# Kernel optimization log

Measured on AMD Instinct MI355X. Metric: run time of the kernel, lower is better.

## Reference

```python
import jax, jax.numpy as jnp
import numpy as np

N = 16384       # num_nodes
IN = 128        # in_features
OUT = 128       # out_features
E = 524288      # num edges
NG = 8          # FastKAN num_grids
GRID_MIN, GRID_MAX = -2.0, 2.0
LN_EPS = 1e-5


def setup_inputs() -> dict:
    key = jax.random.key(0)
    ks = jax.random.split(key, 6)
    x = jax.random.normal(ks[0], (N, IN), dtype=jnp.float32)
    edge_index = jax.random.randint(ks[1], (2, E), 0, N, dtype=jnp.int32)
    # FastKANLayer params
    ln_gamma = jnp.ones((IN,), jnp.float32)
    ln_beta = jnp.zeros((IN,), jnp.float32)
    # SplineLinear: trunc-normal-ish init with scale 0.1 (fast-kan default)
    spline_w = (jax.random.normal(ks[2], (OUT, IN * NG), jnp.float32)
                * (0.1 / np.sqrt(IN * NG)))
    base_w = jax.random.normal(ks[3], (OUT, IN), jnp.float32) / np.sqrt(IN)
    base_b = jnp.zeros((OUT,), jnp.float32)
    # GCNConv.bias
    bias = jax.random.normal(ks[4], (OUT,), jnp.float32) * 0.01
    return dict(x=x, edge_index=edge_index, ln_gamma=ln_gamma, ln_beta=ln_beta,
                spline_w=spline_w, base_w=base_w, base_b=base_b, bias=bias)


def _fastkan(x, ln_gamma, ln_beta, spline_w, base_w, base_b):
    # LayerNorm
    mu = jnp.mean(x, axis=-1, keepdims=True)
    var = jnp.mean((x - mu) ** 2, axis=-1, keepdims=True)
    h = (x - mu) * jax.lax.rsqrt(var + LN_EPS) * ln_gamma + ln_beta
    # Gaussian RBF basis over fixed grid
    grid = jnp.linspace(GRID_MIN, GRID_MAX, NG)
    denom = (GRID_MAX - GRID_MIN) / (NG - 1)
    basis = jnp.exp(-(((h[..., None] - grid) / denom) ** 2))  # [N, IN, NG]
    out = basis.reshape(x.shape[0], IN * NG) @ spline_w.T      # [N, OUT]
    out = out + jax.nn.silu(x) @ base_w.T + base_b             # base update
    return out


def reference(x, edge_index, ln_gamma, ln_beta, spline_w, base_w, base_b, bias):
    num_nodes = x.shape[0]
    # Dense symmetric adjacency, exactly as the torch module builds it
    adj = jnp.zeros((num_nodes, num_nodes), x.dtype)
    adj = adj.at[edge_index[0], edge_index[1]].set(1.0)
    adj = adj.at[edge_index[1], edge_index[0]].set(1.0)
    deg = jnp.sum(adj, axis=1)
    dis = 1.0 / jnp.sqrt(deg)
    norm_adj = adj * dis[:, None] * dis[None, :]
    support = _fastkan(x, ln_gamma, ln_beta, spline_w, base_w, base_b)
    return norm_adj @ support + bias
```

## Files before the change

kernel.cpp:

```cpp
#include <hip/hip_runtime.h>

#define N_NODES 16384
#define NE 524288
#define KDIM 1152
#define KPAD 1160
#define KSTEPS 36
#define NBUCK 512
#define SBLK 512
#define SPB 2048
#define MROW 516
#define DCAP 256

typedef unsigned int uint32;
typedef unsigned short ushort;
typedef __attribute__((ext_vector_type(8))) short bf16x8;
typedef __attribute__((ext_vector_type(4))) float f32x4;

__device__ __forceinline__ ushort f2bf(float f) {
    unsigned u = __float_as_uint(f);
    unsigned r = (u + 0x7fffu + ((u >> 16) & 1u)) >> 16;
    return (ushort)r;
}
__device__ __forceinline__ float bflo(uint32 u) {
    return __uint_as_float(u << 16);
}
__device__ __forceinline__ float bfhi(uint32 u) {
    return __uint_as_float(u & 0xffff0000u);
}

__global__ __launch_bounds__(256) void pre_kernel(
    const int* __restrict__ ei, uint32* __restrict__ ebuf,
    uint32* __restrict__ ocnt, const float* __restrict__ sw,
    const float* __restrict__ bw, ushort* __restrict__ Wp) {
    const int t = threadIdx.x;
    if (blockIdx.x >= SBLK) {
        int idx = (blockIdx.x - SBLK) * 256 + t;
        int i  = idx & 7;
        int l  = (idx >> 3) & 63;
        int ct = (idx >> 9) & 7;
        int kk = idx >> 12;
        int k   = kk * 32 + ((l >> 4) << 3) + i;
        int col = ct * 16 + (l & 15);
        float v = (k < 1024) ? sw[col * 1024 + k] : bw[col * 128 + (k - 1024)];
        Wp[idx] = f2bf(v);
        return;
    }
    __shared__ int hcnt[NBUCK];
    __shared__ int lbase[NBUCK];
    __shared__ uint32 st[SPB];
    hcnt[t] = 0;
    hcnt[t + 256] = 0;
    __syncthreads();

    int bk[8], sl[8];
    uint32 pk[8];
#pragma unroll
    for (int k = 0; k < 4; ++k) {
        int e = blockIdx.x * 1024 + k * 256 + t;
        int a = ei[e];
        int b = ei[NE + e];
        bk[2 * k]     = a >> 5;
        pk[2 * k]     = ((uint32)(a & 31) << 14) | (uint32)b;
        bk[2 * k + 1] = b >> 5;
        pk[2 * k + 1] = ((uint32)(b & 31) << 14) | (uint32)a;
        sl[2 * k]     = atomicAdd(&hcnt[bk[2 * k]], 1);
        sl[2 * k + 1] = atomicAdd(&hcnt[bk[2 * k + 1]], 1);
    }
    __syncthreads();

    const int c0 = hcnt[t];
    const int c1 = hcnt[t + 256];
    for (int off = 1; off < NBUCK; off <<= 1) {
        int v0 = hcnt[t], v1 = hcnt[t + 256];
        int a0 = (t >= off) ? hcnt[t - off] : 0;
        int a1 = hcnt[t + 256 - off];
        __syncthreads();
        hcnt[t] = v0 + a0;
        hcnt[t + 256] = v1 + a1;
        __syncthreads();
    }
    const int e0 = hcnt[t] - c0;
    const int e1 = hcnt[t + 256] - c1;
    lbase[t] = e0;
    lbase[t + 256] = e1;
    uint32* oc = ocnt + (size_t)blockIdx.x * NBUCK;
    oc[t]       = (uint32)e0 | ((uint32)c0 << 16);
    oc[t + 256] = (uint32)e1 | ((uint32)c1 << 16);
    __syncthreads();

#pragma unroll
    for (int k = 0; k < 8; ++k) st[lbase[bk[k]] + sl[k]] = pk[k];
    __syncthreads();
    uint32* gout = ebuf + (size_t)blockIdx.x * SPB;
#pragma unroll
    for (int k = 0; k < 8; ++k) gout[t + k * 256] = st[t + k * 256];
}

__global__ __launch_bounds__(256) void mid_kernel(
    const uint32* __restrict__ ebuf, const uint32* __restrict__ ocnt,
    float* __restrict__ dis, int* __restrict__ degarr,
    ushort* __restrict__ dadj, const float* __restrict__ x,
    const float* __restrict__ gamma, const float* __restrict__ beta,
    const ushort* __restrict__ Wp, const float* __restrict__ base_b,
    ushort* __restrict__ S) {
    __shared__ __align__(16) uint32 smemw[18560];
    const int t = threadIdx.x;
    const int lane = t & 63;
    const int w = t >> 6;

    if (blockIdx.x < NBUCK) {
        uint32* mask = smemw;
        const int bkt = blockIdx.x;
        for (int i = t; i < 32 * MROW; i += 256) mask[i] = 0;
        __syncthreads();

        for (int b = t; b < SBLK; b += 256) {
            uint32 oc = ocnt[(size_t)b * NBUCK + bkt];
            int off = (int)(oc & 0xFFFFu);
            int cn  = (int)(oc >> 16);
            const uint32* p = ebuf + (size_t)b * SPB + off;
            for (int s = 0; s < cn; ++s) {
                uint32 e = p[s];
                atomicOr(&mask[(e >> 14) * MROW + ((e & 16383) >> 5)],
                         1u << (e & 31));
            }
        }
        __syncthreads();

        for (int n = w * 8; n < w * 8 + 8; ++n) {
            const uint32* row = &mask[n * MROW];
            uint32 wd[8];
            int c = 0;
#pragma unroll
            for (int j = 0; j < 8; ++j) {
                wd[j] = row[lane + 64 * j];
                c += __popc(wd[j]);
            }
            int inc = c;
#pragma unroll
            for (int o = 1; o < 64; o <<= 1) {
                int v = __shfl_up(inc, o);
                if (lane >= o) inc += v;
            }
            int total = __shfl(inc, 63);
            int pos = inc - c;
            const int node = bkt * 32 + n;
            if (lane == 0) {
                dis[node] = rsqrtf((float)total);
                degarr[node] = total > DCAP ? DCAP : total;
            }
            ushort* drow = dadj + (size_t)node * DCAP;
#pragma unroll
            for (int j = 0; j < 8; ++j) {
                uint32 bits = wd[j];
                int base = (lane + 64 * j) * 32;
                while (bits) {
                    int b = __ffs(bits) - 1;
                    bits &= bits - 1;
                    if (pos < DCAP) drow[pos] = (ushort)(base + b);
                    ++pos;
                }
            }
        }
        return;
    }

    ushort* Bs = (ushort*)smemw;
    const int nodeBase = (blockIdx.x - NBUCK) * 32;

    const float g0 = gamma[lane], g1 = gamma[lane + 64];
    const float be0 = beta[lane], be1 = beta[lane + 64];

    for (int n = w * 8; n < w * 8 + 8; ++n) {
        const int row = nodeBase + n;
        float f0 = x[(size_t)row * 128 + lane];
        float f1 = x[(size_t)row * 128 + lane + 64];
        float s = f0 + f1;
#pragma unroll
        for (int o = 32; o; o >>= 1) s += __shfl_xor(s, o);
        float mu = s * 0.0078125f;
        float d0 = f0 - mu, d1 = f1 - mu;
        float v = d0 * d0 + d1 * d1;
#pragma unroll
        for (int o = 32; o; o >>= 1) v += __shfl_xor(v, o);
        float rstd = rsqrtf(v * 0.0078125f + 1e-5f);
        float h0 = d0 * rstd * g0 + be0;
        float h1 = d1 * rstd * g1 + be1;
        ushort pk0[8] __attribute__((aligned(16)));
        ushort pk1[8] __attribute__((aligned(16)));
#pragma unroll
        for (int g = 0; g < 8; ++g) {
            float gv = -2.0f + (float)g * (4.0f / 7.0f);
            float z0 = (h0 - gv) * 1.75f;
            float z1 = (h1 - gv) * 1.75f;
            pk0[g] = f2bf(__expf(-z0 * z0));
            pk1[g] = f2bf(__expf(-z1 * z1));
        }
        *reinterpret_cast<uint4*>(&Bs[n * KPAD + lane * 8]) =
            *reinterpret_cast<const uint4*>(pk0);
        *reinterpret_cast<uint4*>(&Bs[n * KPAD + (lane + 64) * 8]) =
            *reinterpret_cast<const uint4*>(pk1);
        Bs[n * KPAD + 1024 + lane]      = f2bf(f0 / (1.0f + __expf(-f0)));
        Bs[n * KPAD + 1024 + lane + 64] = f2bf(f1 / (1.0f + __expf(-f1)));
    }
    __syncthreads();

    const int ct0 = w * 2;
    f32x4 accA = {0.f, 0.f, 0.f, 0.f};
    f32x4 accB = {0.f, 0.f, 0.f, 0.f};
    f32x4 accC = {0.f, 0.f, 0.f, 0.f};
    f32x4 accD = {0.f, 0.f, 0.f, 0.f};
    const ushort* Alo = &Bs[(lane & 15) * KPAD + (lane >> 4) * 8];
    const ushort* Ahi = Alo + 16 * KPAD;
    const bf16x8* Wv = (const bf16x8*)Wp;
#pragma unroll 4
    for (int kk = 0; kk < KSTEPS; ++kk) {
        bf16x8 alo = *reinterpret_cast<const bf16x8*>(Alo + kk * 32);
        bf16x8 ahi = *reinterpret_cast<const bf16x8*>(Ahi + kk * 32);
        bf16x8 b0 = Wv[(size_t)(kk * 8 + ct0) * 64 + lane];
        bf16x8 b1 = Wv[(size_t)(kk * 8 + ct0 + 1) * 64 + lane];
        accA = __builtin_amdgcn_mfma_f32_16x16x32_bf16(alo, b0, accA, 0, 0, 0);
        accB = __builtin_amdgcn_mfma_f32_16x16x32_bf16(alo, b1, accB, 0, 0, 0);
        accC = __builtin_amdgcn_mfma_f32_16x16x32_bf16(ahi, b0, accC, 0, 0, 0);
        accD = __builtin_amdgcn_mfma_f32_16x16x32_bf16(ahi, b1, accD, 0, 0, 0);
    }

    const int col0 = ct0 * 16 + (lane & 15);
    const int rbase = (lane >> 4) * 4;
    const float bb0 = base_b[col0];
    const float bb1 = base_b[col0 + 16];
#pragma unroll
    for (int r = 0; r < 4; ++r) {
        const int rlo = nodeBase + rbase + r;
        const int rhi = rlo + 16;
        S[(size_t)rlo * 128 + col0]      = f2bf(accA[r] + bb0);
        S[(size_t)rlo * 128 + col0 + 16] = f2bf(accB[r] + bb1);
        S[(size_t)rhi * 128 + col0]      = f2bf(accC[r] + bb0);
        S[(size_t)rhi * 128 + col0 + 16] = f2bf(accD[r] + bb1);
    }
}

__global__ __launch_bounds__(256) void aggregate_kernel(
    const int* __restrict__ degarr, const ushort* __restrict__ dadj,
    const ushort* __restrict__ S, const float* __restrict__ dis,
    const float* __restrict__ bias, float* __restrict__ out) {
    __shared__ ushort lst[2][DCAP];
    __shared__ float part[2][2][128];
    const int t = threadIdx.x;
    const int g = t >> 7;
    const int tl = t & 127;
    const int i = blockIdx.x * 2 + g;

    const int total = degarr[i];
    const ushort* drow = dadj + (size_t)i * DCAP;
    if (tl < total) lst[g][tl] = drow[tl];
    if (tl + 128 < total) lst[g][tl + 128] = drow[tl + 128];
    __syncthreads();

    const int lane = t & 63;
    const int wv = (t >> 6) & 1;
    const uint32* S32 = (const uint32*)S;
    float a0 = 0.f, a1 = 0.f;
    int idx = wv;
    for (; idx + 6 < total; idx += 8) {
        int j0 = lst[g][idx], j1 = lst[g][idx + 2];
        int j2 = lst[g][idx + 4], j3 = lst[g][idx + 6];
        float d0 = dis[j0], d1 = dis[j1], d2 = dis[j2], d3 = dis[j3];
        uint32 u0 = S32[(size_t)j0 * 64 + lane];
        uint32 u1 = S32[(size_t)j1 * 64 + lane];
        uint32 u2 = S32[(size_t)j2 * 64 + lane];
        uint32 u3 = S32[(size_t)j3 * 64 + lane];
        a0 += (d0 * bflo(u0) + d1 * bflo(u1)) + (d2 * bflo(u2) + d3 * bflo(u3));
        a1 += (d0 * bfhi(u0) + d1 * bfhi(u1)) + (d2 * bfhi(u2) + d3 * bfhi(u3));
    }
    for (; idx < total; idx += 2) {
        int j = lst[g][idx];
        float d = dis[j];
        uint32 u = S32[(size_t)j * 64 + lane];
        a0 += d * bflo(u);
        a1 += d * bfhi(u);
    }
    part[g][wv][lane * 2]     = a0;
    part[g][wv][lane * 2 + 1] = a1;
    __syncthreads();

    float v = part[g][0][tl] + part[g][1][tl];
    out[(size_t)i * 128 + tl] = v * dis[i] + bias[tl];
}

extern "C" void kernel_launch(void* const* d_in, const int* in_sizes, int n_in,
                              void* d_out, int out_size, void* d_ws, size_t ws_size,
                              hipStream_t stream) {
    const float* x        = (const float*)d_in[0];
    const int*   ei       = (const int*)d_in[1];
    const float* ln_gamma = (const float*)d_in[2];
    const float* ln_beta  = (const float*)d_in[3];
    const float* spline_w = (const float*)d_in[4];
    const float* base_w   = (const float*)d_in[5];
    const float* base_b   = (const float*)d_in[6];
    const float* bias     = (const float*)d_in[7];
    float* out = (float*)d_out;

    char* ws = (char*)d_ws;
    const size_t WP_OFF   = 0;
    const size_t DIS_OFF  = 294912;
    const size_t DEG_OFF  = 360448;
    const size_t DADJ_OFF = 425984;
    const size_t EBUF_OFF = 8814592;
    const size_t OCNT_OFF = 13008896;
    const size_t S_OFF    = 14057472;
    const size_t NEEDED   = 18251776;
    if (ws_size < NEEDED) return;

    ushort* Wp     = (ushort*)(ws + WP_OFF);
    float*  dis    = (float*)(ws + DIS_OFF);
    int*    degarr = (int*)(ws + DEG_OFF);
    ushort* dadj   = (ushort*)(ws + DADJ_OFF);
    uint32* ebuf   = (uint32*)(ws + EBUF_OFF);
    uint32* ocnt   = (uint32*)(ws + OCNT_OFF);
    ushort* S      = (ushort*)(ws + S_OFF);

    pre_kernel<<<SBLK + 576, 256, 0, stream>>>(ei, ebuf, ocnt,
                                               spline_w, base_w, Wp);
    mid_kernel<<<NBUCK + N_NODES / 32, 256, 0, stream>>>(
        ebuf, ocnt, dis, degarr, dadj, x, ln_gamma, ln_beta, Wp, base_b, S);
    aggregate_kernel<<<N_NODES / 2, 256, 0, stream>>>(degarr, dadj, S, dis,
                                                      bias, out);
}
```

Before: 78.16 us.

## Replace per-block edge bucketing with global counting-sort scatter into contiguous buckets

The edge bucketing is reworked into a global counting sort. A count kernel, a per-bucket prefix-scan kernel and a scatter kernel write edges into contiguous per-bucket regions of fixed capacity, so the degree kernel reads one contiguous range instead of gathering 512 small segments. The scatter is fused into the same launch as the FastKAN GEMM, which now uses 16-node tiles to raise block count and lower shared memory per block. This adds two extra kernel launches and uncoalesced global scatter writes, and silently drops edges if a bucket exceeds its fixed capacity.

```diff
diff --git a/kernel.cpp b/kernel.cpp
--- a/kernel.cpp
+++ b/kernel.cpp
@@ -7,7 +7,7 @@
 #define KSTEPS 36
 #define NBUCK 512
 #define SBLK 512
-#define SPB 2048
+#define BCAP2 2816
 #define MROW 516
 #define DCAP 256
 
@@ -28,10 +28,10 @@
     return __uint_as_float(u & 0xffff0000u);
 }
 
-__global__ __launch_bounds__(256) void pre_kernel(
-    const int* __restrict__ ei, uint32* __restrict__ ebuf,
-    uint32* __restrict__ ocnt, const float* __restrict__ sw,
-    const float* __restrict__ bw, ushort* __restrict__ Wp) {
+__global__ __launch_bounds__(256) void preA_kernel(
+    const int* __restrict__ ei, uint32* __restrict__ cntT,
+    const float* __restrict__ sw, const float* __restrict__ bw,
+    ushort* __restrict__ Wp) {
     const int t = threadIdx.x;
     if (blockIdx.x >= SBLK) {
         int idx = (blockIdx.x - SBLK) * 256 + t;
@@ -46,132 +46,97 @@
         return;
     }
     __shared__ int hcnt[NBUCK];
-    __shared__ int lbase[NBUCK];
-    __shared__ uint32 st[SPB];
     hcnt[t] = 0;
     hcnt[t + 256] = 0;
     __syncthreads();
-
-    int bk[8], sl[8];
-    uint32 pk[8];
 #pragma unroll
     for (int k = 0; k < 4; ++k) {
         int e = blockIdx.x * 1024 + k * 256 + t;
         int a = ei[e];
         int b = ei[NE + e];
-        bk[2 * k]     = a >> 5;
-        pk[2 * k]     = ((uint32)(a & 31) << 14) | (uint32)b;
-        bk[2 * k + 1] = b >> 5;
-        pk[2 * k + 1] = ((uint32)(b & 31) << 14) | (uint32)a;
-        sl[2 * k]     = atomicAdd(&hcnt[bk[2 * k]], 1);
-        sl[2 * k + 1] = atomicAdd(&hcnt[bk[2 * k + 1]], 1);
-    }
-    __syncthreads();
-
-    const int c0 = hcnt[t];
-    const int c1 = hcnt[t + 256];
-    for (int off = 1; off < NBUCK; off <<= 1) {
-        int v0 = hcnt[t], v1 = hcnt[t + 256];
-        int a0 = (t >= off) ? hcnt[t - off] : 0;
-        int a1 = hcnt[t + 256 - off];
+        atomicAdd(&hcnt[a >> 5], 1);
+        atomicAdd(&hcnt[b >> 5], 1);
+    }
+    __syncthreads();
+    cntT[(size_t)t * SBLK + blockIdx.x]         = (uint32)hcnt[t];
+    cntT[(size_t)(t + 256) * SBLK + blockIdx.x] = (uint32)hcnt[t + 256];
+}
+
+__global__ __launch_bounds__(256) void preB_kernel(
+    const uint32* __restrict__ cntT, uint32* __restrict__ pos,
+    uint32* __restrict__ bsize) {
+    __shared__ int sc[SBLK];
+    const int t = threadIdx.x;
+    const int q = blockIdx.x;
+    sc[t]       = (int)cntT[(size_t)q * SBLK + t];
+    sc[t + 256] = (int)cntT[(size_t)q * SBLK + t + 256];
+    __syncthreads();
+    const int c0 = sc[t];
+    const int c1 = sc[t + 256];
+    for (int off = 1; off < SBLK; off <<= 1) {
+        int v0 = sc[t], v1 = sc[t + 256];
+        int a0 = (t >= off) ? sc[t - off] : 0;
+        int a1 = sc[t + 256 - off];
         __syncthreads();
-        hcnt[t] = v0 + a0;
-        hcnt[t + 256] = v1 + a1;
+        sc[t] = v0 + a0;
+        sc[t + 256] = v1 + a1;
         __syncthreads();
     }
-    const int e0 = hcnt[t] - c0;
-    const int e1 = hcnt[t + 256] - c1;
-    lbase[t] = e0;
-    lbase[t + 256] = e1;
-    uint32* oc = ocnt + (size_t)blockIdx.x * NBUCK;
-    oc[t]       = (uint32)e0 | ((uint32)c0 << 16);
-    oc[t + 256] = (uint32)e1 | ((uint32)c1 << 16);
-    __syncthreads();
-
-#pragma unroll
-    for (int k = 0; k < 8; ++k) st[lbase[bk[k]] + sl[k]] = pk[k];
-    __syncthreads();
-    uint32* gout = ebuf + (size_t)blockIdx.x * SPB;
-#pragma unroll
-    for (int k = 0; k < 8; ++k) gout[t + k * 256] = st[t + k * 256];
-}
-
-__global__ __launch_bounds__(256) void mid_kernel(
-    const uint32* __restrict__ ebuf, const uint32* __restrict__ ocnt,
-    float* __restrict__ dis, int* __restrict__ degarr,
-    ushort* __restrict__ dadj, const float* __restrict__ x,
+    const uint32 base = (uint32)q * BCAP2;
+    pos[(size_t)t * NBUCK + q]         = base + (uint32)(sc[t] - c0);
+    pos[(size_t)(t + 256) * NBUCK + q] = base + (uint32)(sc[t + 256] - c1);
+    if (t == 0) {
+        int total = sc[511];
+        bsize[q] = (uint32)(total > BCAP2 ? BCAP2 : total);
+    }
+}
+
+__global__ __launch_bounds__(256) void midC_kernel(
+    const int* __restrict__ ei, const uint32* __restrict__ pos,
+    uint32* __restrict__ ebuf, const float* __restrict__ x,
     const float* __restrict__ gamma, const float* __restrict__ beta,
     const ushort* __restrict__ Wp, const float* __restrict__ base_b,
     ushort* __restrict__ S) {
-    __shared__ __align__(16) uint32 smemw[18560];
+    __shared__ __align__(16) ushort smem[16 * KPAD];
     const int t = threadIdx.x;
     const int lane = t & 63;
     const int w = t >> 6;
 
-    if (blockIdx.x < NBUCK) {
-        uint32* mask = smemw;
-        const int bkt = blockIdx.x;
-        for (int i = t; i < 32 * MROW; i += 256) mask[i] = 0;
+    if (blockIdx.x < SBLK) {
+        int* hcnt = (int*)smem;
+        uint32* lpos = (uint32*)smem + NBUCK;
+        const int b = blockIdx.x;
+        lpos[t]       = pos[(size_t)b * NBUCK + t];
+        lpos[t + 256] = pos[(size_t)b * NBUCK + t + 256];
+        hcnt[t] = 0;
+        hcnt[t + 256] = 0;
         __syncthreads();
-
-        for (int b = t; b < SBLK; b += 256) {
-            uint32 oc = ocnt[(size_t)b * NBUCK + bkt];
-            int off = (int)(oc & 0xFFFFu);
-            int cn  = (int)(oc >> 16);
-            const uint32* p = ebuf + (size_t)b * SPB + off;
-            for (int s = 0; s < cn; ++s) {
-                uint32 e = p[s];
-                atomicOr(&mask[(e >> 14) * MROW + ((e & 16383) >> 5)],
-                         1u << (e & 31));
-            }
-        }
-        __syncthreads();
-
-        for (int n = w * 8; n < w * 8 + 8; ++n) {
-            const uint32* row = &mask[n * MROW];
-            uint32 wd[8];
-            int c = 0;
-#pragma unroll
-            for (int j = 0; j < 8; ++j) {
-                wd[j] = row[lane + 64 * j];
-                c += __popc(wd[j]);
-            }
-            int inc = c;
-#pragma unroll
-            for (int o = 1; o < 64; o <<= 1) {
-                int v = __shfl_up(inc, o);
-                if (lane >= o) inc += v;
-            }
-            int total = __shfl(inc, 63);
-            int pos = inc - c;
-            const int node = bkt * 32 + n;
-            if (lane == 0) {
-                dis[node] = rsqrtf((float)total);
-                degarr[node] = total > DCAP ? DCAP : total;
-            }
-            ushort* drow = dadj + (size_t)node * DCAP;
-#pragma unroll
-            for (int j = 0; j < 8; ++j) {
-                uint32 bits = wd[j];
-                int base = (lane + 64 * j) * 32;
-                while (bits) {
-                    int b = __ffs(bits) - 1;
-                    bits &= bits - 1;
-                    if (pos < DCAP) drow[pos] = (ushort)(base + b);
-                    ++pos;
-                }
-            }
+#pragma unroll
+        for (int k = 0; k < 4; ++k) {
+            int e = b * 1024 + k * 256 + t;
+            int a = ei[e];
+            int bb = ei[NE + e];
+            int qa = a >> 5;
+            int sl = atomicAdd(&hcnt[qa], 1);
+            uint32 idx = lpos[qa] + (uint32)sl;
+            if (idx < (uint32)(qa + 1) * BCAP2)
+                ebuf[idx] = ((uint32)(a & 31) << 14) | (uint32)bb;
+            int qb = bb >> 5;
+            sl = atomicAdd(&hcnt[qb], 1);
+            idx = lpos[qb] + (uint32)sl;
+            if (idx < (uint32)(qb + 1) * BCAP2)
+                ebuf[idx] = ((uint32)(bb & 31) << 14) | (uint32)a;
         }
         return;
     }
 
-    ushort* Bs = (ushort*)smemw;
-    const int nodeBase = (blockIdx.x - NBUCK) * 32;
+    ushort* Bs = smem;
+    const int nodeBase = (blockIdx.x - SBLK) * 16;
 
     const float g0 = gamma[lane], g1 = gamma[lane + 64];
     const float be0 = beta[lane], be1 = beta[lane + 64];
 
-    for (int n = w * 8; n < w * 8 + 8; ++n) {
+    for (int n = w * 4; n < w * 4 + 4; ++n) {
         const int row = nodeBase + n;
         float f0 = x[(size_t)row * 128 + lane];
         float f1 = x[(size_t)row * 128 + lane + 64];
@@ -206,23 +171,17 @@
     __syncthreads();
 
     const int ct0 = w * 2;
-    f32x4 accA = {0.f, 0.f, 0.f, 0.f};
-    f32x4 accB = {0.f, 0.f, 0.f, 0.f};
-    f32x4 accC = {0.f, 0.f, 0.f, 0.f};
-    f32x4 accD = {0.f, 0.f, 0.f, 0.f};
-    const ushort* Alo = &Bs[(lane & 15) * KPAD + (lane >> 4) * 8];
-    const ushort* Ahi = Alo + 16 * KPAD;
+    f32x4 acc0 = {0.f, 0.f, 0.f, 0.f};
+    f32x4 acc1 = {0.f, 0.f, 0.f, 0.f};
+    const ushort* ArowBase = &Bs[(lane & 15) * KPAD + (lane >> 4) * 8];
     const bf16x8* Wv = (const bf16x8*)Wp;
 #pragma unroll 4
     for (int kk = 0; kk < KSTEPS; ++kk) {
-        bf16x8 alo = *reinterpret_cast<const bf16x8*>(Alo + kk * 32);
-        bf16x8 ahi = *reinterpret_cast<const bf16x8*>(Ahi + kk * 32);
+        bf16x8 a = *reinterpret_cast<const bf16x8*>(ArowBase + kk * 32);
         bf16x8 b0 = Wv[(size_t)(kk * 8 + ct0) * 64 + lane];
         bf16x8 b1 = Wv[(size_t)(kk * 8 + ct0 + 1) * 64 + lane];
-        accA = __builtin_amdgcn_mfma_f32_16x16x32_bf16(alo, b0, accA, 0, 0, 0);
-        accB = __builtin_amdgcn_mfma_f32_16x16x32_bf16(alo, b1, accB, 0, 0, 0);
-        accC = __builtin_amdgcn_mfma_f32_16x16x32_bf16(ahi, b0, accC, 0, 0, 0);
-        accD = __builtin_amdgcn_mfma_f32_16x16x32_bf16(ahi, b1, accD, 0, 0, 0);
+        acc0 = __builtin_amdgcn_mfma_f32_16x16x32_bf16(a, b0, acc0, 0, 0, 0);
+        acc1 = __builtin_amdgcn_mfma_f32_16x16x32_bf16(a, b1, acc1, 0, 0, 0);
     }
 
     const int col0 = ct0 * 16 + (lane & 15);
@@ -231,12 +190,66 @@
     const float bb1 = base_b[col0 + 16];
 #pragma unroll
     for (int r = 0; r < 4; ++r) {
-        const int rlo = nodeBase + rbase + r;
-        const int rhi = rlo + 16;
-        S[(size_t)rlo * 128 + col0]      = f2bf(accA[r] + bb0);
-        S[(size_t)rlo * 128 + col0 + 16] = f2bf(accB[r] + bb1);
-        S[(size_t)rhi * 128 + col0]      = f2bf(accC[r] + bb0);
-        S[(size_t)rhi * 128 + col0 + 16] = f2bf(accD[r] + bb1);
+        const int row = nodeBase + rbase + r;
+        S[(size_t)row * 128 + col0]      = f2bf(acc0[r] + bb0);
+        S[(size_t)row * 128 + col0 + 16] = f2bf(acc1[r] + bb1);
+    }
+}
+
+__global__ __launch_bounds__(256) void degb_kernel(
+    const uint32* __restrict__ ebuf, const uint32* __restrict__ bsize,
+    float* __restrict__ dis, int* __restrict__ degarr,
+    ushort* __restrict__ dadj) {
+    __shared__ uint32 mask[32 * MROW];
+    const int t = threadIdx.x;
+    const int bkt = blockIdx.x;
+    for (int i = t; i < 32 * MROW; i += 256) mask[i] = 0;
+    __syncthreads();
+
+    const int n = (int)bsize[bkt];
+    const uint32* p = ebuf + (size_t)bkt * BCAP2;
+    for (int idx = t; idx < n; idx += 256) {
+        uint32 e = p[idx];
+        atomicOr(&mask[(e >> 14) * MROW + ((e & 16383) >> 5)], 1u << (e & 31));
+    }
+    __syncthreads();
+
+    const int lane = t & 63;
+    const int w = t >> 6;
+    for (int nn = w * 8; nn < w * 8 + 8; ++nn) {
+        const uint32* row = &mask[nn * MROW];
+        uint32 wd[8];
+        int c = 0;
+#pragma unroll
+        for (int j = 0; j < 8; ++j) {
+            wd[j] = row[lane + 64 * j];
+            c += __popc(wd[j]);
+        }
+        int inc = c;
+#pragma unroll
+        for (int o = 1; o < 64; o <<= 1) {
+            int v = __shfl_up(inc, o);
+            if (lane >= o) inc += v;
+        }
+        int total = __shfl(inc, 63);
+        int ppos = inc - c;
+        const int node = bkt * 32 + nn;
+        if (lane == 0) {
+            dis[node] = rsqrtf((float)total);
+            degarr[node] = total > DCAP ? DCAP : total;
+        }
+        ushort* drow = dadj + (size_t)node * DCAP;
+#pragma unroll
+        for (int j = 0; j < 8; ++j) {
+            uint32 bits = wd[j];
+            int base = (lane + 64 * j) * 32;
+            while (bits) {
+                int b = __ffs(bits) - 1;
+                bits &= bits - 1;
+                if (ppos < DCAP) drow[ppos] = (ushort)(base + b);
+                ++ppos;
+            }
+        }
     }
 }
 
@@ -306,24 +319,29 @@
     const size_t DIS_OFF  = 294912;
     const size_t DEG_OFF  = 360448;
     const size_t DADJ_OFF = 425984;
-    const size_t EBUF_OFF = 8814592;
-    const size_t OCNT_OFF = 13008896;
-    const size_t S_OFF    = 14057472;
-    const size_t NEEDED   = 18251776;
+    const size_t CNTT_OFF = 8814592;
+    const size_t POS_OFF  = 9863168;
+    const size_t BSZ_OFF  = 10911744;
+    const size_t EBUF_OFF = 10915840;
+    const size_t S_OFF    = 16683008;
+    const size_t NEEDED   = 20877312;
     if (ws_size < NEEDED) return;
 
     ushort* Wp     = (ushort*)(ws + WP_OFF);
     float*  dis    = (float*)(ws + DIS_OFF);
     int*    degarr = (int*)(ws + DEG_OFF);
     ushort* dadj   = (ushort*)(ws + DADJ_OFF);
+    uint32* cntT   = (uint32*)(ws + CNTT_OFF);
+    uint32* pos    = (uint32*)(ws + POS_OFF);
+    uint32* bsize  = (uint32*)(ws + BSZ_OFF);
     uint32* ebuf   = (uint32*)(ws + EBUF_OFF);
-    uint32* ocnt   = (uint32*)(ws + OCNT_OFF);
     ushort* S      = (ushort*)(ws + S_OFF);
 
-    pre_kernel<<<SBLK + 576, 256, 0, stream>>>(ei, ebuf, ocnt,
-                                               spline_w, base_w, Wp);
-    mid_kernel<<<NBUCK + N_NODES / 32, 256, 0, stream>>>(
-        ebuf, ocnt, dis, degarr, dadj, x, ln_gamma, ln_beta, Wp, base_b, S);
+    preA_kernel<<<SBLK + 576, 256, 0, stream>>>(ei, cntT, spline_w, base_w, Wp);
+    preB_kernel<<<NBUCK, 256, 0, stream>>>(cntT, pos, bsize);
+    midC_kernel<<<SBLK + N_NODES / 16, 256, 0, stream>>>(
+        ei, pos, ebuf, x, ln_gamma, ln_beta, Wp, base_b, S);
+    degb_kernel<<<NBUCK, 256, 0, stream>>>(ebuf, bsize, dis, degarr, dadj);
     aggregate_kernel<<<N_NODES / 2, 256, 0, stream>>>(degarr, dadj, S, dis,
                                                       bias, out);
 }
```

Result: slower. 85.07 us (+8.8%).

## Halve per-block work in mid kernel and interleave bucket and GEMM blocks

Applied to the files above, without the earlier changes.

Doubles the number of edge buckets so each adjacency block handles 16 nodes instead of 32, and each GEMM block computes 16 rows instead of 32. Shared memory per block drops from about 74KB to about 37KB, which should allow more resident blocks per CU. Bucket blocks and GEMM blocks now alternate by block index, so the two workload types overlap on the device. The prefix scan in the pre kernel is rewritten to handle 1024 buckets. The cost is that each bucket block now reads ocnt entries from all 512 source blocks for half as many nodes, and each GEMM block has half the MFMA work per W load.

```diff
diff --git a/kernel.cpp b/kernel.cpp
--- a/kernel.cpp
+++ b/kernel.cpp
@@ -5,7 +5,7 @@
 #define KDIM 1152
 #define KPAD 1160
 #define KSTEPS 36
-#define NBUCK 512
+#define NBUCK 1024
 #define SBLK 512
 #define SPB 2048
 #define MROW 516
@@ -47,9 +47,9 @@
     }
     __shared__ int hcnt[NBUCK];
     __shared__ int lbase[NBUCK];
+    __shared__ int ps[256];
     __shared__ uint32 st[SPB];
-    hcnt[t] = 0;
-    hcnt[t + 256] = 0;
+    for (int q = t; q < NBUCK; q += 256) hcnt[q] = 0;
     __syncthreads();
 
     int bk[8], sl[8];
@@ -59,33 +59,40 @@
         int e = blockIdx.x * 1024 + k * 256 + t;
         int a = ei[e];
         int b = ei[NE + e];
-        bk[2 * k]     = a >> 5;
-        pk[2 * k]     = ((uint32)(a & 31) << 14) | (uint32)b;
-        bk[2 * k + 1] = b >> 5;
-        pk[2 * k + 1] = ((uint32)(b & 31) << 14) | (uint32)a;
+        bk[2 * k]     = a >> 4;
+        pk[2 * k]     = ((uint32)(a & 15) << 14) | (uint32)b;
+        bk[2 * k + 1] = b >> 4;
+        pk[2 * k + 1] = ((uint32)(b & 15) << 14) | (uint32)a;
         sl[2 * k]     = atomicAdd(&hcnt[bk[2 * k]], 1);
         sl[2 * k + 1] = atomicAdd(&hcnt[bk[2 * k + 1]], 1);
     }
     __syncthreads();
 
-    const int c0 = hcnt[t];
-    const int c1 = hcnt[t + 256];
-    for (int off = 1; off < NBUCK; off <<= 1) {
-        int v0 = hcnt[t], v1 = hcnt[t + 256];
-        int a0 = (t >= off) ? hcnt[t - off] : 0;
-        int a1 = hcnt[t + 256 - off];
+    int c[4], loc[4];
+    int s = 0;
+#pragma unroll
+    for (int q = 0; q < 4; ++q) {
+        c[q] = hcnt[t * 4 + q];
+        loc[q] = s;
+        s += c[q];
+    }
+    ps[t] = s;
+    __syncthreads();
+    for (int off = 1; off < 256; off <<= 1) {
+        int v = ps[t];
+        int add = (t >= off) ? ps[t - off] : 0;
         __syncthreads();
-        hcnt[t] = v0 + a0;
-        hcnt[t + 256] = v1 + a1;
+        ps[t] = v + add;
         __syncthreads();
     }
-    const int e0 = hcnt[t] - c0;
-    const int e1 = hcnt[t + 256] - c1;
-    lbase[t] = e0;
-    lbase[t + 256] = e1;
+    const int base = (t == 0) ? 0 : ps[t - 1];
     uint32* oc = ocnt + (size_t)blockIdx.x * NBUCK;
-    oc[t]       = (uint32)e0 | ((uint32)c0 << 16);
-    oc[t + 256] = (uint32)e1 | ((uint32)c1 << 16);
+#pragma unroll
+    for (int q = 0; q < 4; ++q) {
+        int e0 = base + loc[q];
+        lbase[t * 4 + q] = e0;
+        oc[t * 4 + q] = (uint32)e0 | ((uint32)c[q] << 16);
+    }
     __syncthreads();
 
 #pragma unroll
@@ -103,15 +110,15 @@
     const float* __restrict__ gamma, const float* __restrict__ beta,
     const ushort* __restrict__ Wp, const float* __restrict__ base_b,
     ushort* __restrict__ S) {
-    __shared__ __align__(16) uint32 smemw[18560];
+    __shared__ __align__(16) ushort smem[16 * KPAD];
     const int t = threadIdx.x;
     const int lane = t & 63;
     const int w = t >> 6;
 
-    if (blockIdx.x < NBUCK) {
-        uint32* mask = smemw;
-        const int bkt = blockIdx.x;
-        for (int i = t; i < 32 * MROW; i += 256) mask[i] = 0;
+    if (blockIdx.x & 1) {
+        uint32* mask = (uint32*)smem;
+        const int bkt = blockIdx.x >> 1;
+        for (int i = t; i < 16 * MROW; i += 256) mask[i] = 0;
         __syncthreads();
 
         for (int b = t; b < SBLK; b += 256) {
@@ -127,7 +134,7 @@
         }
         __syncthreads();
 
-        for (int n = w * 8; n < w * 8 + 8; ++n) {
+        for (int n = w * 4; n < w * 4 + 4; ++n) {
             const uint32* row = &mask[n * MROW];
             uint32 wd[8];
             int c = 0;
@@ -144,7 +151,7 @@
             }
             int total = __shfl(inc, 63);
             int pos = inc - c;
-            const int node = bkt * 32 + n;
+            const int node = bkt * 16 + n;
             if (lane == 0) {
                 dis[node] = rsqrtf((float)total);
                 degarr[node] = total > DCAP ? DCAP : total;
@@ -165,13 +172,13 @@
         return;
     }
 
-    ushort* Bs = (ushort*)smemw;
-    const int nodeBase = (blockIdx.x - NBUCK) * 32;
+    ushort* Bs = smem;
+    const int nodeBase = (blockIdx.x >> 1) * 16;
 
     const float g0 = gamma[lane], g1 = gamma[lane + 64];
     const float be0 = beta[lane], be1 = beta[lane + 64];
 
-    for (int n = w * 8; n < w * 8 + 8; ++n) {
+    for (int n = w * 4; n < w * 4 + 4; ++n) {
         const int row = nodeBase + n;
         float f0 = x[(size_t)row * 128 + lane];
         float f1 = x[(size_t)row * 128 + lane + 64];
@@ -206,23 +213,17 @@
     __syncthreads();
 
     const int ct0 = w * 2;
-    f32x4 accA = {0.f, 0.f, 0.f, 0.f};
-    f32x4 accB = {0.f, 0.f, 0.f, 0.f};
-    f32x4 accC = {0.f, 0.f, 0.f, 0.f};
-    f32x4 accD = {0.f, 0.f, 0.f, 0.f};
-    const ushort* Alo = &Bs[(lane & 15) * KPAD + (lane >> 4) * 8];
-    const ushort* Ahi = Alo + 16 * KPAD;
+    f32x4 acc0 = {0.f, 0.f, 0.f, 0.f};
+    f32x4 acc1 = {0.f, 0.f, 0.f, 0.f};
+    const ushort* ArowBase = &Bs[(lane & 15) * KPAD + (lane >> 4) * 8];
     const bf16x8* Wv = (const bf16x8*)Wp;
 #pragma unroll 4
     for (int kk = 0; kk < KSTEPS; ++kk) {
-        bf16x8 alo = *reinterpret_cast<const bf16x8*>(Alo + kk * 32);
-        bf16x8 ahi = *reinterpret_cast<const bf16x8*>(Ahi + kk * 32);
+        bf16x8 a = *reinterpret_cast<const bf16x8*>(ArowBase + kk * 32);
         bf16x8 b0 = Wv[(size_t)(kk * 8 + ct0) * 64 + lane];
         bf16x8 b1 = Wv[(size_t)(kk * 8 + ct0 + 1) * 64 + lane];
-        accA = __builtin_amdgcn_mfma_f32_16x16x32_bf16(alo, b0, accA, 0, 0, 0);
-        accB = __builtin_amdgcn_mfma_f32_16x16x32_bf16(alo, b1, accB, 0, 0, 0);
-        accC = __builtin_amdgcn_mfma_f32_16x16x32_bf16(ahi, b0, accC, 0, 0, 0);
-        accD = __builtin_amdgcn_mfma_f32_16x16x32_bf16(ahi, b1, accD, 0, 0, 0);
+        acc0 = __builtin_amdgcn_mfma_f32_16x16x32_bf16(a, b0, acc0, 0, 0, 0);
+        acc1 = __builtin_amdgcn_mfma_f32_16x16x32_bf16(a, b1, acc1, 0, 0, 0);
     }
 
     const int col0 = ct0 * 16 + (lane & 15);
@@ -231,12 +232,9 @@
     const float bb1 = base_b[col0 + 16];
 #pragma unroll
     for (int r = 0; r < 4; ++r) {
-        const int rlo = nodeBase + rbase + r;
-        const int rhi = rlo + 16;
-        S[(size_t)rlo * 128 + col0]      = f2bf(accA[r] + bb0);
-        S[(size_t)rlo * 128 + col0 + 16] = f2bf(accB[r] + bb1);
-        S[(size_t)rhi * 128 + col0]      = f2bf(accC[r] + bb0);
-        S[(size_t)rhi * 128 + col0 + 16] = f2bf(accD[r] + bb1);
+        const int row = nodeBase + rbase + r;
+        S[(size_t)row * 128 + col0]      = f2bf(acc0[r] + bb0);
+        S[(size_t)row * 128 + col0 + 16] = f2bf(acc1[r] + bb1);
     }
 }
 
@@ -306,24 +304,24 @@
     const size_t DIS_OFF  = 294912;
     const size_t DEG_OFF  = 360448;
     const size_t DADJ_OFF = 425984;
-    const size_t EBUF_OFF = 8814592;
-    const size_t OCNT_OFF = 13008896;
-    const size_t S_OFF    = 14057472;
-    const size_t NEEDED   = 18251776;
+    const size_t OCNT_OFF = 8814592;
+    const size_t EBUF_OFF = 10911744;
+    const size_t S_OFF    = 15106048;
+    const size_t NEEDED   = 19300352;
     if (ws_size < NEEDED) return;
 
     ushort* Wp     = (ushort*)(ws + WP_OFF);
     float*  dis    = (float*)(ws + DIS_OFF);
     int*    degarr = (int*)(ws + DEG_OFF);
     ushort* dadj   = (ushort*)(ws + DADJ_OFF);
+    uint32* ocnt   = (uint32*)(ws + OCNT_OFF);
     uint32* ebuf   = (uint32*)(ws + EBUF_OFF);
-    uint32* ocnt   = (uint32*)(ws + OCNT_OFF);
     ushort* S      = (ushort*)(ws + S_OFF);
 
     pre_kernel<<<SBLK + 576, 256, 0, stream>>>(ei, ebuf, ocnt,
                                                spline_w, base_w, Wp);
-    mid_kernel<<<NBUCK + N_NODES / 32, 256, 0, stream>>>(
-        ebuf, ocnt, dis, degarr, dadj, x, ln_gamma, ln_beta, Wp, base_b, S);
+    mid_kernel<<<2048, 256, 0, stream>>>(ebuf, ocnt, dis, degarr, dadj,
+                                         x, ln_gamma, ln_beta, Wp, base_b, S);
     aggregate_kernel<<<N_NODES / 2, 256, 0, stream>>>(degarr, dadj, S, dis,
                                                       bias, out);
 }
```

New measurement: 68.80 us. 1.14x faster.
